# Kernel optimization log

Measured on AMD Instinct MI355X. Metric: run time of the kernel, lower is better.

The kernel has to match this reference:

```python
import jax, jax.numpy as jnp
import numpy as np

START_IDX = 1  # Offsets.GO
END_IDX = 2    # Offsets.EOS
NEG_INF = -10000.0


def setup_inputs() -> dict:
    key = jax.random.key(0)
    k1, k2, k3 = jax.random.split(key, 3)
    B, T, N = 256, 1024, 128
    unary = jax.random.normal(k1, (B, T, N), dtype=jnp.float32)
    trans = jax.random.normal(k2, (1, N, N), dtype=jnp.float32) * 0.1
    lengths = jax.random.randint(k3, (B,), 1, T + 1)
    return {"unary": unary, "trans": trans, "lengths": lengths}


def _forward_alg(unary_btn, trans, lengths):
    """CRF log-partition. unary_btn: [B,T,N], trans: [1,N,N], lengths: [B] -> [B]."""
    B, T, N = unary_btn.shape
    tr = trans[0]  # [N(cur), N(prev)]
    unary_tbn = jnp.transpose(unary_btn, (1, 0, 2))  # batch_first -> [T,B,N]

    init_alphas = jnp.full((B, N), NEG_INF, dtype=unary_btn.dtype)
    init_alphas = init_alphas.at[:, START_IDX].set(0.0)

    def step(alphas, inp):
        unary_t, t = inp  # unary_t: [B,N]
        # scores[b, i, j] = alphas[b, j] + trans[i, j] + unary_t[b, i]
        scores = alphas[:, None, :] + tr[None, :, :] + unary_t[:, :, None]
        new_alphas = jax.nn.logsumexp(scores, axis=2)  # [B,N]
        # only advance positions still inside the sequence
        alphas = jnp.where((t < lengths)[:, None], new_alphas, alphas)
        return alphas, None

    alphas, _ = jax.lax.scan(step, init_alphas, (unary_tbn, jnp.arange(T)))
    terminal = alphas + tr[END_IDX][None, :]  # trans[:, end_idx] row: [N]
    return jax.nn.logsumexp(terminal, axis=1)  # [B]


def reference(unary, trans, lengths):
    return _forward_alg(unary, trans, lengths)
```

## Files before the change

### kernel.cpp

```cpp
#include <hip/hip_runtime.h>

#define T_LEN 1024
#define NS    128
#define BT    16
#define G     16
#define SEG   32
#define SSH   5
#define NB    256

typedef __attribute__((ext_vector_type(8))) short short8;
typedef __attribute__((ext_vector_type(4))) short short4v;
typedef __attribute__((ext_vector_type(4))) float f32x4;

static __device__ __forceinline__ short f2bf(float f) {
    unsigned u = __builtin_bit_cast(unsigned, f);
    u = (u + 0x7fffu + ((u >> 16) & 1u)) >> 16;
    return (short)u;
}
static __device__ __forceinline__ float bf2f(short s) {
    unsigned u = ((unsigned)(unsigned short)s) << 16;
    return __builtin_bit_cast(float, u);
}
static __device__ __forceinline__ short f2bf_trunc(float f) {
    return (short)(__builtin_bit_cast(unsigned, f) >> 16);
}

__global__ __launch_bounds__(256, 1) void crf_seg(
        const float* __restrict__ unary, const float* __restrict__ trans,
        const int* __restrict__ lengths,
        float* __restrict__ yv, float* __restrict__ zv,
        float* __restrict__ cfv, float* __restrict__ cbv) {
    __shared__ __align__(16) short Fs[2][BT * NS];
    __shared__ __align__(16) float Us[2][BT * NS];
    __shared__ int tbS[BT], teS[BT];
    __shared__ int itersS;

    const int tid = threadIdx.x;
    const int g = blockIdx.x & (G - 1);
    const int u = blockIdx.x >> 4;
    const bool bwd = u >= (SEG - 1);
    const int s = bwd ? (u - (SEG - 2)) : u;
    const int w = tid >> 6, lane = tid & 63;
    const int quad = lane >> 4, bcol = lane & 15;
    const int sr = tid >> 4, sc = tid & 15;

    if (tid == 0) itersS = 0;
    if (tid < BT) {
        int L = lengths[g * BT + tid];
        tbS[tid] = (s * L) >> SSH;
        teS[tid] = ((s + 1) * L) >> SSH;
    }
    __syncthreads();
    if (tid < BT) atomicMax(&itersS, teS[tid] - tbS[tid]);

    const int tb = tbS[bcol], te = teS[bcol];
    const int nrec = te - tb - 1;
    const int s_tb = tbS[sr], s_te = teS[sr];

    short8 Ea[2][4];
    #pragma unroll
    for (int mt = 0; mt < 2; ++mt) {
        const int i = w * 32 + mt * 16 + bcol;
        #pragma unroll
        for (int kt = 0; kt < 4; ++kt) {
            short8 e;
            if (!bwd) {
                const float* tr = trans + (size_t)i * NS + kt * 32 + quad * 8;
                float4 x = *(const float4*)tr, y = *(const float4*)(tr + 4);
                e[0] = f2bf(__expf(x.x)); e[1] = f2bf(__expf(x.y));
                e[2] = f2bf(__expf(x.z)); e[3] = f2bf(__expf(x.w));
                e[4] = f2bf(__expf(y.x)); e[5] = f2bf(__expf(y.y));
                e[6] = f2bf(__expf(y.z)); e[7] = f2bf(__expf(y.w));
            } else {
                #pragma unroll
                for (int jj = 0; jj < 8; ++jj)
                    e[jj] = f2bf(__expf(trans[(size_t)(kt * 32 + quad * 8 + jj) * NS + i]));
            }
            Ea[mt][kt] = e;
        }
    }

    const float* ubase = unary + (size_t)(g * BT + sr) * T_LEN * NS + sc * 8;

    {
        float v[8];
        if (!bwd) {
            #pragma unroll
            for (int k = 0; k < 8; ++k)
                v[k] = (s == 0) ? ((sc * 8 + k == 1) ? 1.f : 0.f) : 1.f;
        } else {
            int ti = s_te - 1; if (ti < 0) ti = 0;
            const float* up = ubase + (size_t)ti * NS;
            float4 ua = *(const float4*)up, ub4 = *(const float4*)(up + 4);
            float uu[8] = {ua.x, ua.y, ua.z, ua.w, ub4.x, ub4.y, ub4.z, ub4.w};
            #pragma unroll
            for (int k = 0; k < 8; ++k) {
                float vv = (s == SEG - 1) ? __expf(trans[2 * NS + sc * 8 + k]) : 1.f;
                v[k] = __expf(uu[k]) * vv;
            }
        }
        short8 z;
        #pragma unroll
        for (int k = 0; k < 8; ++k) z[k] = f2bf(v[k]);
        *(short8*)&Fs[0][sr * NS + ((sc ^ sr) << 3)] = z;

        if (s_te == s_tb) {
            if (!bwd) {
                float* yp = yv + ((size_t)s * NB + g * BT + sr) * NS + sc * 8;
                #pragma unroll
                for (int k = 0; k < 8; ++k)
                    yp[k] = (s == 0) ? ((sc * 8 + k == 1) ? 1.f : 0.f) : 1.f;
                if (sc == 0) cfv[s * NB + g * BT + sr] = 0.f;
            } else {
                float* zp = zv + ((size_t)(s - 1) * NB + g * BT + sr) * NS + sc * 8;
                #pragma unroll
                for (int k = 0; k < 8; ++k) zp[k] = 1.f;
                if (sc == 0) cbv[(s - 1) * NB + g * BT + sr] = 0.f;
            }
        }
    }

    const int u_off0 = sr * NS + (((2 * sc) ^ (sr & 7)) << 2);
    const int u_off1 = sr * NS + (((2 * sc + 1) ^ (sr & 7)) << 2);
    #define T_OF(n) ({ int _t = bwd ? (s_te - 2 - (n)) : (s_tb + (n)); \
                       _t = _t < 0 ? 0 : (_t > T_LEN - 1 ? T_LEN - 1 : _t); _t; })
    float4 ra0, ra1;
    {
        int t = T_OF(0);
        ra0 = *(const float4*)(ubase + (size_t)t * NS);
        ra1 = *(const float4*)(ubase + (size_t)t * NS + 4);
        *(float4*)&Us[0][u_off0] = ra0;
        *(float4*)&Us[0][u_off1] = ra1;
        t = T_OF(1);
        ra0 = *(const float4*)(ubase + (size_t)t * NS);
        ra1 = *(const float4*)(ubase + (size_t)t * NS + 4);
    }
    __syncthreads();
    const int iters = itersS;

    int bfOff[4];
    #pragma unroll
    for (int kt = 0; kt < 4; ++kt) bfOff[kt] = bcol * NS + (((kt * 4 + quad) ^ bcol) << 3);
    const int s4Off = bcol * NS + (bcol << 3);
    const int ur0 = bcol * NS + (((w * 8 + quad) ^ (bcol & 7)) << 2);
    const int ur1 = bcol * NS + (((w * 8 + 4 + quad) ^ (bcol & 7)) << 2);
    const int c0 = w * 4 + (quad >> 1), half = (quad & 1) << 2;
    const int fw0 = bcol * NS + ((c0 ^ bcol) << 3) + half;
    const int fw1 = bcol * NS + (((c0 + 2) ^ bcol) << 3) + half;

    float C = 0.f;
    for (int n = 0; n < iters; ++n) {
        const int cur = n & 1, nxt = cur ^ 1;
        const short* fb = Fs[cur];
        short8 Bf0 = *(const short8*)&fb[bfOff[0]];
        short8 Bf1 = *(const short8*)&fb[bfOff[1]];
        short8 Bf2 = *(const short8*)&fb[bfOff[2]];
        short8 Bf3 = *(const short8*)&fb[bfOff[3]];
        short4v s4 = *(const short4v*)&fb[s4Off];
        float4 u0 = *(const float4*)&Us[cur][ur0];
        float4 u1 = *(const float4*)&Us[cur][ur1];

        *(float4*)&Us[nxt][u_off0] = ra0;
        *(float4*)&Us[nxt][u_off1] = ra1;
        {
            int t = T_OF(n + 2);
            ra0 = *(const float4*)(ubase + (size_t)t * NS);
            ra1 = *(const float4*)(ubase + (size_t)t * NS + 4);
        }

        f32x4 x0 = {0.f,0.f,0.f,0.f}, y0 = {0.f,0.f,0.f,0.f};
        f32x4 x1 = {0.f,0.f,0.f,0.f}, y1 = {0.f,0.f,0.f,0.f};
        x0 = __builtin_amdgcn_mfma_f32_16x16x32_bf16(Ea[0][0], Bf0, x0, 0, 0, 0);
        x1 = __builtin_amdgcn_mfma_f32_16x16x32_bf16(Ea[1][0], Bf0, x1, 0, 0, 0);
        y0 = __builtin_amdgcn_mfma_f32_16x16x32_bf16(Ea[0][2], Bf2, y0, 0, 0, 0);
        y1 = __builtin_amdgcn_mfma_f32_16x16x32_bf16(Ea[1][2], Bf2, y1, 0, 0, 0);
        x0 = __builtin_amdgcn_mfma_f32_16x16x32_bf16(Ea[0][1], Bf1, x0, 0, 0, 0);
        x1 = __builtin_amdgcn_mfma_f32_16x16x32_bf16(Ea[1][1], Bf1, x1, 0, 0, 0);
        y0 = __builtin_amdgcn_mfma_f32_16x16x32_bf16(Ea[0][3], Bf3, y0, 0, 0, 0);
        y1 = __builtin_amdgcn_mfma_f32_16x16x32_bf16(Ea[1][3], Bf3, y1, 0, 0, 0);
        f32x4 a0 = x0 + y0, a1 = x1 + y1;

        float sv = (bf2f(s4[0]) + bf2f(s4[1])) + (bf2f(s4[2]) + bf2f(s4[3]));
        float rs = __fdividef(1.f, sv);
        float logs = __logf(sv);
        float e0[4], e1[4];
        e0[0] = __expf(u0.x); e0[1] = __expf(u0.y); e0[2] = __expf(u0.z); e0[3] = __expf(u0.w);
        e1[0] = __expf(u1.x); e1[1] = __expf(u1.y); e1[2] = __expf(u1.z); e1[3] = __expf(u1.w);
        float fn0[4], fn1[4];
        #pragma unroll
        for (int r = 0; r < 4; ++r) {
            fn0[r] = a0[r] * e0[r] * rs;
            fn1[r] = a1[r] * e1[r] * rs;
        }

        if (n == nrec) {
            if (!bwd) {
                float* yp = yv + ((size_t)s * NB + g * BT + bcol) * NS;
                *(float4*)(yp + w * 32 + quad * 4)      = (float4){fn0[0], fn0[1], fn0[2], fn0[3]};
                *(float4*)(yp + w * 32 + 16 + quad * 4) = (float4){fn1[0], fn1[1], fn1[2], fn1[3]};
                if (tid < BT) cfv[s * NB + g * BT + tid] = C + logs;
            } else {
                float* zp = zv + ((size_t)(s - 1) * NB + g * BT + bcol) * NS;
                *(float4*)(zp + w * 32 + quad * 4)      = (float4){a0[0], a0[1], a0[2], a0[3]};
                *(float4*)(zp + w * 32 + 16 + quad * 4) = (float4){a1[0], a1[1], a1[2], a1[3]};
                if (tid < BT) cbv[(s - 1) * NB + g * BT + tid] = C;
            }
        }
        C += logs;

        short4v p0, p1;
        #pragma unroll
        for (int r = 0; r < 4; ++r) { p0[r] = f2bf_trunc(fn0[r]); p1[r] = f2bf_trunc(fn1[r]); }
        *(short4v*)&Fs[nxt][fw0] = p0;
        *(short4v*)&Fs[nxt][fw1] = p1;

        asm volatile("s_waitcnt lgkmcnt(0)" ::: "memory");
        __builtin_amdgcn_s_barrier();
    }
}

__global__ __launch_bounds__(64) void crf_combine(
        const float* __restrict__ yv, const float* __restrict__ zv,
        const float* __restrict__ cfv, const float* __restrict__ cbv,
        float* __restrict__ out) {
    const int b = blockIdx.x, lane = threadIdx.x;
    float acc = cfv[b];
    for (int s = 1; s <= SEG - 1; ++s) acc += cbv[(s - 1) * NB + b];
    float lg = 0.f;
    for (int s = 1; s <= SEG - 1; ++s) {
        const float* Z = zv + ((size_t)(s - 1) * NB + b) * NS;
        const float* Y = yv + ((size_t)(s - 1) * NB + b) * NS;
        float d = Z[lane] * Y[lane] + Z[lane + 64] * Y[lane + 64];
        #pragma unroll
        for (int off = 1; off < 64; off <<= 1) d += __shfl_xor(d, off, 64);
        lg += __logf(d);
    }
    for (int s = 1; s <= SEG - 2; ++s) {
        const float* Y = yv + ((size_t)s * NB + b) * NS;
        float t = Y[lane] + Y[lane + 64];
        #pragma unroll
        for (int off = 1; off < 64; off <<= 1) t += __shfl_xor(t, off, 64);
        lg -= __logf(t);
    }
    if (lane == 0) out[b] = acc + lg;
}

extern "C" void kernel_launch(void* const* d_in, const int* in_sizes, int n_in,
                              void* d_out, int out_size, void* d_ws, size_t ws_size,
                              hipStream_t stream) {
    const float* unary   = (const float*)d_in[0];
    const float* trans   = (const float*)d_in[1];
    const int*   lengths = (const int*)d_in[2];
    float* out = (float*)d_out;

    float* yv  = (float*)d_ws;
    float* zv  = yv + (size_t)(SEG - 1) * NB * NS;
    float* cfv = zv + (size_t)(SEG - 1) * NB * NS;
    float* cbv = cfv + (size_t)(SEG - 1) * NB;

    crf_seg<<<dim3(2 * (SEG - 1) * G), dim3(256), 0, stream>>>(
        unary, trans, lengths, yv, zv, cfv, cbv);
    crf_combine<<<dim3(NB), dim3(64), 0, stream>>>(yv, zv, cfv, cbv, out);
}
```

Baseline: 231.4 us.

## Load unary directly into MFMA output layout, dropping LDS staging buffer

New measurement: 228.9 us. No clear change (-1.1%).

```diff
diff --git a/kernel.cpp b/kernel.cpp
--- a/kernel.cpp
+++ b/kernel.cpp
@@ -25,13 +25,12 @@
     return (short)(__builtin_bit_cast(unsigned, f) >> 16);
 }
 
-__global__ __launch_bounds__(256, 1) void crf_seg(
+__global__ __launch_bounds__(256, 4) void crf_seg(
         const float* __restrict__ unary, const float* __restrict__ trans,
         const int* __restrict__ lengths,
         float* __restrict__ yv, float* __restrict__ zv,
         float* __restrict__ cfv, float* __restrict__ cbv) {
     __shared__ __align__(16) short Fs[2][BT * NS];
-    __shared__ __align__(16) float Us[2][BT * NS];
     __shared__ int tbS[BT], teS[BT];
     __shared__ int itersS;
 
@@ -80,9 +79,8 @@
         }
     }
 
-    const float* ubase = unary + (size_t)(g * BT + sr) * T_LEN * NS + sc * 8;
-
     {
+        const float* ubase = unary + (size_t)(g * BT + sr) * T_LEN * NS + sc * 8;
         float v[8];
         if (!bwd) {
             #pragma unroll
@@ -120,21 +118,16 @@
         }
     }
 
-    const int u_off0 = sr * NS + (((2 * sc) ^ (sr & 7)) << 2);
-    const int u_off1 = sr * NS + (((2 * sc + 1) ^ (sr & 7)) << 2);
-    #define T_OF(n) ({ int _t = bwd ? (s_te - 2 - (n)) : (s_tb + (n)); \
-                       _t = _t < 0 ? 0 : (_t > T_LEN - 1 ? T_LEN - 1 : _t); _t; })
-    float4 ra0, ra1;
-    {
-        int t = T_OF(0);
-        ra0 = *(const float4*)(ubase + (size_t)t * NS);
-        ra1 = *(const float4*)(ubase + (size_t)t * NS + 4);
-        *(float4*)&Us[0][u_off0] = ra0;
-        *(float4*)&Us[0][u_off1] = ra1;
-        t = T_OF(1);
-        ra0 = *(const float4*)(ubase + (size_t)t * NS);
-        ra1 = *(const float4*)(ubase + (size_t)t * NS + 4);
-    }
+    const float* uptr = unary + (size_t)(g * BT + bcol) * T_LEN * NS + (w * 32 + quad * 4);
+    #define T_OFB(nn) ({ int _t = bwd ? (te - 2 - (nn)) : (tb + (nn)); \
+                         _t = _t < 0 ? 0 : (_t > T_LEN - 1 ? T_LEN - 1 : _t); _t; })
+    float4 pA0, pA1, pB0, pB1;
+    { int t = T_OFB(0);
+      pA0 = *(const float4*)(uptr + (size_t)t * NS);
+      pA1 = *(const float4*)(uptr + (size_t)t * NS + 16); }
+    { int t = T_OFB(1);
+      pB0 = *(const float4*)(uptr + (size_t)t * NS);
+      pB1 = *(const float4*)(uptr + (size_t)t * NS + 16); }
     __syncthreads();
     const int iters = itersS;
 
@@ -142,81 +135,80 @@
     #pragma unroll
     for (int kt = 0; kt < 4; ++kt) bfOff[kt] = bcol * NS + (((kt * 4 + quad) ^ bcol) << 3);
     const int s4Off = bcol * NS + (bcol << 3);
-    const int ur0 = bcol * NS + (((w * 8 + quad) ^ (bcol & 7)) << 2);
-    const int ur1 = bcol * NS + (((w * 8 + 4 + quad) ^ (bcol & 7)) << 2);
     const int c0 = w * 4 + (quad >> 1), half = (quad & 1) << 2;
     const int fw0 = bcol * NS + ((c0 ^ bcol) << 3) + half;
     const int fw1 = bcol * NS + (((c0 + 2) ^ bcol) << 3) + half;
 
     float C = 0.f;
-    for (int n = 0; n < iters; ++n) {
-        const int cur = n & 1, nxt = cur ^ 1;
-        const short* fb = Fs[cur];
-        short8 Bf0 = *(const short8*)&fb[bfOff[0]];
-        short8 Bf1 = *(const short8*)&fb[bfOff[1]];
-        short8 Bf2 = *(const short8*)&fb[bfOff[2]];
-        short8 Bf3 = *(const short8*)&fb[bfOff[3]];
-        short4v s4 = *(const short4v*)&fb[s4Off];
-        float4 u0 = *(const float4*)&Us[cur][ur0];
-        float4 u1 = *(const float4*)&Us[cur][ur1];
-
-        *(float4*)&Us[nxt][u_off0] = ra0;
-        *(float4*)&Us[nxt][u_off1] = ra1;
-        {
-            int t = T_OF(n + 2);
-            ra0 = *(const float4*)(ubase + (size_t)t * NS);
-            ra1 = *(const float4*)(ubase + (size_t)t * NS + 4);
-        }
-
-        f32x4 x0 = {0.f,0.f,0.f,0.f}, y0 = {0.f,0.f,0.f,0.f};
-        f32x4 x1 = {0.f,0.f,0.f,0.f}, y1 = {0.f,0.f,0.f,0.f};
-        x0 = __builtin_amdgcn_mfma_f32_16x16x32_bf16(Ea[0][0], Bf0, x0, 0, 0, 0);
-        x1 = __builtin_amdgcn_mfma_f32_16x16x32_bf16(Ea[1][0], Bf0, x1, 0, 0, 0);
-        y0 = __builtin_amdgcn_mfma_f32_16x16x32_bf16(Ea[0][2], Bf2, y0, 0, 0, 0);
-        y1 = __builtin_amdgcn_mfma_f32_16x16x32_bf16(Ea[1][2], Bf2, y1, 0, 0, 0);
-        x0 = __builtin_amdgcn_mfma_f32_16x16x32_bf16(Ea[0][1], Bf1, x0, 0, 0, 0);
-        x1 = __builtin_amdgcn_mfma_f32_16x16x32_bf16(Ea[1][1], Bf1, x1, 0, 0, 0);
-        y0 = __builtin_amdgcn_mfma_f32_16x16x32_bf16(Ea[0][3], Bf3, y0, 0, 0, 0);
-        y1 = __builtin_amdgcn_mfma_f32_16x16x32_bf16(Ea[1][3], Bf3, y1, 0, 0, 0);
-        f32x4 a0 = x0 + y0, a1 = x1 + y1;
-
-        float sv = (bf2f(s4[0]) + bf2f(s4[1])) + (bf2f(s4[2]) + bf2f(s4[3]));
-        float rs = __fdividef(1.f, sv);
-        float logs = __logf(sv);
-        float e0[4], e1[4];
-        e0[0] = __expf(u0.x); e0[1] = __expf(u0.y); e0[2] = __expf(u0.z); e0[3] = __expf(u0.w);
-        e1[0] = __expf(u1.x); e1[1] = __expf(u1.y); e1[2] = __expf(u1.z); e1[3] = __expf(u1.w);
-        float fn0[4], fn1[4];
-        #pragma unroll
-        for (int r = 0; r < 4; ++r) {
-            fn0[r] = a0[r] * e0[r] * rs;
-            fn1[r] = a1[r] * e1[r] * rs;
-        }
-
-        if (n == nrec) {
-            if (!bwd) {
-                float* yp = yv + ((size_t)s * NB + g * BT + bcol) * NS;
-                *(float4*)(yp + w * 32 + quad * 4)      = (float4){fn0[0], fn0[1], fn0[2], fn0[3]};
-                *(float4*)(yp + w * 32 + 16 + quad * 4) = (float4){fn1[0], fn1[1], fn1[2], fn1[3]};
-                if (tid < BT) cfv[s * NB + g * BT + tid] = C + logs;
-            } else {
-                float* zp = zv + ((size_t)(s - 1) * NB + g * BT + bcol) * NS;
-                *(float4*)(zp + w * 32 + quad * 4)      = (float4){a0[0], a0[1], a0[2], a0[3]};
-                *(float4*)(zp + w * 32 + 16 + quad * 4) = (float4){a1[0], a1[1], a1[2], a1[3]};
-                if (tid < BT) cbv[(s - 1) * NB + g * BT + tid] = C;
-            }
-        }
-        C += logs;
-
-        short4v p0, p1;
-        #pragma unroll
-        for (int r = 0; r < 4; ++r) { p0[r] = f2bf_trunc(fn0[r]); p1[r] = f2bf_trunc(fn1[r]); }
-        *(short4v*)&Fs[nxt][fw0] = p0;
-        *(short4v*)&Fs[nxt][fw1] = p1;
-
-        asm volatile("s_waitcnt lgkmcnt(0)" ::: "memory");
-        __builtin_amdgcn_s_barrier();
-    }
+
+#define STEP(U0, U1) do {                                                         \
+    const int cur = n & 1, nxt = cur ^ 1;                                         \
+    const short* fb = Fs[cur];                                                    \
+    short8 Bf0 = *(const short8*)&fb[bfOff[0]];                                   \
+    short8 Bf1 = *(const short8*)&fb[bfOff[1]];                                   \
+    short8 Bf2 = *(const short8*)&fb[bfOff[2]];                                   \
+    short8 Bf3 = *(const short8*)&fb[bfOff[3]];                                   \
+    short4v s4 = *(const short4v*)&fb[s4Off];                                     \
+    float e0[4], e1[4];                                                           \
+    e0[0] = __expf(U0.x); e0[1] = __expf(U0.y);                                   \
+    e0[2] = __expf(U0.z); e0[3] = __expf(U0.w);                                   \
+    e1[0] = __expf(U1.x); e1[1] = __expf(U1.y);                                   \
+    e1[2] = __expf(U1.z); e1[3] = __expf(U1.w);                                   \
+    { int t = T_OFB(n + 2);                                                       \
+      U0 = *(const float4*)(uptr + (size_t)t * NS);                               \
+      U1 = *(const float4*)(uptr + (size_t)t * NS + 16); }                        \
+    f32x4 x0 = {0.f,0.f,0.f,0.f}, y0 = {0.f,0.f,0.f,0.f};                         \
+    f32x4 x1 = {0.f,0.f,0.f,0.f}, y1 = {0.f,0.f,0.f,0.f};                         \
+    x0 = __builtin_amdgcn_mfma_f32_16x16x32_bf16(Ea[0][0], Bf0, x0, 0, 0, 0);     \
+    x1 = __builtin_amdgcn_mfma_f32_16x16x32_bf16(Ea[1][0], Bf0, x1, 0, 0, 0);     \
+    y0 = __builtin_amdgcn_mfma_f32_16x16x32_bf16(Ea[0][2], Bf2, y0, 0, 0, 0);     \
+    y1 = __builtin_amdgcn_mfma_f32_16x16x32_bf16(Ea[1][2], Bf2, y1, 0, 0, 0);     \
+    x0 = __builtin_amdgcn_mfma_f32_16x16x32_bf16(Ea[0][1], Bf1, x0, 0, 0, 0);     \
+    x1 = __builtin_amdgcn_mfma_f32_16x16x32_bf16(Ea[1][1], Bf1, x1, 0, 0, 0);     \
+    y0 = __builtin_amdgcn_mfma_f32_16x16x32_bf16(Ea[0][3], Bf3, y0, 0, 0, 0);     \
+    y1 = __builtin_amdgcn_mfma_f32_16x16x32_bf16(Ea[1][3], Bf3, y1, 0, 0, 0);     \
+    f32x4 a0 = x0 + y0, a1 = x1 + y1;                                             \
+    float sv = (bf2f(s4[0]) + bf2f(s4[1])) + (bf2f(s4[2]) + bf2f(s4[3]));         \
+    float rs = __fdividef(1.f, sv);                                               \
+    float logs = __logf(sv);                                                      \
+    float fn0[4], fn1[4];                                                         \
+    fn0[0] = a0[0]*e0[0]*rs; fn0[1] = a0[1]*e0[1]*rs;                             \
+    fn0[2] = a0[2]*e0[2]*rs; fn0[3] = a0[3]*e0[3]*rs;                             \
+    fn1[0] = a1[0]*e1[0]*rs; fn1[1] = a1[1]*e1[1]*rs;                             \
+    fn1[2] = a1[2]*e1[2]*rs; fn1[3] = a1[3]*e1[3]*rs;                             \
+    if (n == nrec) {                                                              \
+        if (!bwd) {              \
+            float* yp = yv + ((size_t)s * NB + g * BT + bcol) * NS;               \
+            *(float4*)(yp + w * 32 + quad * 4)      = (float4){fn0[0], fn0[1], fn0[2], fn0[3]}; \
+            *(float4*)(yp + w * 32 + 16 + quad * 4) = (float4){fn1[0], fn1[1], fn1[2], fn1[3]}; \
+            if (tid < BT) cfv[s * NB + g * BT + tid] = C + logs;                  \
+        } else {                  \
+            float* zp = zv + ((size_t)(s - 1) * NB + g * BT + bcol) * NS;         \
+            *(float4*)(zp + w * 32 + quad * 4)      = (float4){a0[0], a0[1], a0[2], a0[3]}; \
+            *(float4*)(zp + w * 32 + 16 + quad * 4) = (float4){a1[0], a1[1], a1[2], a1[3]}; \
+            if (tid < BT) cbv[(s - 1) * NB + g * BT + tid] = C;                   \
+        }                                                                         \
+    }                                                                             \
+    C += logs;                                                                    \
+    short4v p0, p1;                                                               \
+    p0[0] = f2bf_trunc(fn0[0]); p0[1] = f2bf_trunc(fn0[1]);                       \
+    p0[2] = f2bf_trunc(fn0[2]); p0[3] = f2bf_trunc(fn0[3]);                       \
+    p1[0] = f2bf_trunc(fn1[0]); p1[1] = f2bf_trunc(fn1[1]);                       \
+    p1[2] = f2bf_trunc(fn1[2]); p1[3] = f2bf_trunc(fn1[3]);                       \
+    *(short4v*)&Fs[nxt][fw0] = p0;                                                \
+    *(short4v*)&Fs[nxt][fw1] = p1;                                                \
+     \
+    asm volatile("s_waitcnt lgkmcnt(0)" ::: "memory");                            \
+    __builtin_amdgcn_s_barrier();                                                 \
+} while (0)
+
+    for (int n = 0; n < iters; ) {
+        STEP(pA0, pA1); ++n;
+        if (n >= iters) break;
+        STEP(pB0, pB1); ++n;
+    }
+#undef STEP
+#undef T_OFB
 }
 
 __global__ __launch_bounds__(64) void crf_combine(
```

## Split sequence into 128 segments with shared LDS exp(unary) and merged fwd/bwd blocks

Applied to the files above, without the earlier changes.

Measured after the change: 253.7 us. 1.1x slower.

```diff
diff --git a/kernel.cpp b/kernel.cpp
--- a/kernel.cpp
+++ b/kernel.cpp
@@ -4,8 +4,9 @@
 #define NS    128
 #define BT    16
 #define G     16
-#define SEG   32
-#define SSH   5
+#define SEG   128
+#define SSH   7
+#define ST    8
 #define NB    256
 
 typedef __attribute__((ext_vector_type(8))) short short8;
@@ -25,209 +26,270 @@
     return (short)(__builtin_bit_cast(unsigned, f) >> 16);
 }
 
-__global__ __launch_bounds__(256, 1) void crf_seg(
+__global__ __launch_bounds__(256, 4) void crf_seg(
         const float* __restrict__ unary, const float* __restrict__ trans,
         const int* __restrict__ lengths,
         float* __restrict__ yv, float* __restrict__ zv,
         float* __restrict__ cfv, float* __restrict__ cbv) {
-    __shared__ __align__(16) short Fs[2][BT * NS];
-    __shared__ __align__(16) float Us[2][BT * NS];
+    __shared__ __align__(16) short Fs[BT * NS];
+    __shared__ __align__(16) short EU[ST * BT * NS];
     __shared__ int tbS[BT], teS[BT];
-    __shared__ int itersS;
 
     const int tid = threadIdx.x;
     const int g = blockIdx.x & (G - 1);
-    const int u = blockIdx.x >> 4;
-    const bool bwd = u >= (SEG - 1);
-    const int s = bwd ? (u - (SEG - 2)) : u;
+    const int s = blockIdx.x >> 4;
     const int w = tid >> 6, lane = tid & 63;
     const int quad = lane >> 4, bcol = lane & 15;
-    const int sr = tid >> 4, sc = tid & 15;
-
-    if (tid == 0) itersS = 0;
+
     if (tid < BT) {
         int L = lengths[g * BT + tid];
         tbS[tid] = (s * L) >> SSH;
         teS[tid] = ((s + 1) * L) >> SSH;
     }
+    {
+        short8 z = {0, 0, 0, 0, 0, 0, 0, 0};
+        #pragma unroll
+        for (int k = 0; k < 8; ++k) *(short8*)&EU[tid * 64 + k * 8] = z;
+    }
     __syncthreads();
-    if (tid < BT) atomicMax(&itersS, teS[tid] - tbS[tid]);
 
     const int tb = tbS[bcol], te = teS[bcol];
-    const int nrec = te - tb - 1;
-    const int s_tb = tbS[sr], s_te = teS[sr];
-
-    short8 Ea[2][4];
+    const int slen = te - tb;
+    const int nrec = slen - 1;
+    int iters = 0;
     #pragma unroll
-    for (int mt = 0; mt < 2; ++mt) {
-        const int i = w * 32 + mt * 16 + bcol;
-        #pragma unroll
-        for (int kt = 0; kt < 4; ++kt) {
-            short8 e;
-            if (!bwd) {
-                const float* tr = trans + (size_t)i * NS + kt * 32 + quad * 8;
-                float4 x = *(const float4*)tr, y = *(const float4*)(tr + 4);
+    for (int b = 0; b < BT; ++b) {
+        int d = teS[b] - tbS[b];
+        iters = d > iters ? d : iters;
+    }
+    const int slc = slen > 0 ? slen - 1 : 0;
+
+    {
+        const int sb = tid >> 4, rr = (tid >> 1) & 7, hh = tid & 1;
+        const int sl = teS[sb] - tbS[sb];
+        if (rr < sl) {
+            const float* src = unary + ((size_t)(g * BT + sb) * T_LEN + tbS[sb] + rr) * NS + hh * 64;
+            #pragma unroll
+            for (int k8 = 0; k8 < 8; ++k8) {
+                float4 x = *(const float4*)(src + k8 * 8);
+                float4 y = *(const float4*)(src + k8 * 8 + 4);
+                short8 e;
                 e[0] = f2bf(__expf(x.x)); e[1] = f2bf(__expf(x.y));
                 e[2] = f2bf(__expf(x.z)); e[3] = f2bf(__expf(x.w));
                 e[4] = f2bf(__expf(y.x)); e[5] = f2bf(__expf(y.y));
                 e[6] = f2bf(__expf(y.z)); e[7] = f2bf(__expf(y.w));
-            } else {
+                const int c8 = hh * 8 + k8;
+                *(short8*)&EU[rr * (BT * NS) + sb * NS + (((c8 ^ sb) & 15) << 3)] = e;
+            }
+        }
+    }
+
+    short8 Ea[2][4];
+    if (s < SEG - 1) {
+        #pragma unroll
+        for (int mt = 0; mt < 2; ++mt) {
+            const int i = w * 32 + mt * 16 + bcol;
+            #pragma unroll
+            for (int kt = 0; kt < 4; ++kt) {
+                const float* tr = trans + (size_t)i * NS + kt * 32 + quad * 8;
+                float4 x = *(const float4*)tr, y = *(const float4*)(tr + 4);
+                short8 e;
+                e[0] = f2bf(__expf(x.x)); e[1] = f2bf(__expf(x.y));
+                e[2] = f2bf(__expf(x.z)); e[3] = f2bf(__expf(x.w));
+                e[4] = f2bf(__expf(y.x)); e[5] = f2bf(__expf(y.y));
+                e[6] = f2bf(__expf(y.z)); e[7] = f2bf(__expf(y.w));
+                Ea[mt][kt] = e;
+            }
+        }
+    }
+
+    {
+        const int sr = tid >> 4, sc = tid & 15;
+        const int sl = teS[sr] - tbS[sr];
+        short8 z;
+        #pragma unroll
+        for (int k = 0; k < 8; ++k)
+            z[k] = f2bf((s == 0) ? ((sc * 8 + k == 1) ? 1.f : 0.f) : 1.f);
+        *(short8*)&Fs[sr * NS + ((sc ^ sr) << 3)] = z;
+
+        if (sl == 0 && s < SEG - 1) {
+            float* yp = yv + ((size_t)s * NB + g * BT + sr) * NS + sc * 8;
+            #pragma unroll
+            for (int k = 0; k < 8; ++k)
+                yp[k] = (s == 0) ? ((sc * 8 + k == 1) ? 1.f : 0.f) : 1.f;
+            if (sc == 0) cfv[s * NB + g * BT + sr] = 0.f;
+        }
+    }
+    __syncthreads();
+
+    int bfOff[4];
+    #pragma unroll
+    for (int kt = 0; kt < 4; ++kt) bfOff[kt] = bcol * NS + (((kt * 4 + quad) ^ bcol) << 3);
+    const int s4Off = bcol * NS + (bcol << 3);
+    const int c0 = w * 4 + (quad >> 1), halfo = (quad & 1) << 2;
+    const int fw0 = bcol * NS + ((c0 ^ bcol) << 3) + halfo;
+    const int fw1 = bcol * NS + (((c0 + 2) ^ bcol) << 3) + halfo;
+
+#define LGKM_BAR() do { asm volatile("s_waitcnt lgkmcnt(0)" ::: "memory"); \
+                        __builtin_amdgcn_s_barrier(); } while (0)
+
+    if (s < SEG - 1) {
+        float C = 0.f;
+        for (int n = 0; n < iters; ++n) {
+            short8 Bf0 = *(const short8*)&Fs[bfOff[0]];
+            short8 Bf1 = *(const short8*)&Fs[bfOff[1]];
+            short8 Bf2 = *(const short8*)&Fs[bfOff[2]];
+            short8 Bf3 = *(const short8*)&Fs[bfOff[3]];
+            short4v s4 = *(const short4v*)&Fs[s4Off];
+            const int er = n < slen ? n : slc;
+            short4v ev0 = *(const short4v*)&EU[er * (BT * NS) + fw0];
+            short4v ev1 = *(const short4v*)&EU[er * (BT * NS) + fw1];
+            LGKM_BAR();
+
+            float sv = (bf2f(s4[0]) + bf2f(s4[1])) + (bf2f(s4[2]) + bf2f(s4[3]));
+            float rs = __fdividef(1.f, sv);
+            float logs = __logf(sv);
+
+            f32x4 x0 = {0.f,0.f,0.f,0.f}, y0 = {0.f,0.f,0.f,0.f};
+            f32x4 x1 = {0.f,0.f,0.f,0.f}, y1 = {0.f,0.f,0.f,0.f};
+            x0 = __builtin_amdgcn_mfma_f32_16x16x32_bf16(Ea[0][0], Bf0, x0, 0, 0, 0);
+            x1 = __builtin_amdgcn_mfma_f32_16x16x32_bf16(Ea[1][0], Bf0, x1, 0, 0, 0);
+            y0 = __builtin_amdgcn_mfma_f32_16x16x32_bf16(Ea[0][2], Bf2, y0, 0, 0, 0);
+            y1 = __builtin_amdgcn_mfma_f32_16x16x32_bf16(Ea[1][2], Bf2, y1, 0, 0, 0);
+            x0 = __builtin_amdgcn_mfma_f32_16x16x32_bf16(Ea[0][1], Bf1, x0, 0, 0, 0);
+            x1 = __builtin_amdgcn_mfma_f32_16x16x32_bf16(Ea[1][1], Bf1, x1, 0, 0, 0);
+            y0 = __builtin_amdgcn_mfma_f32_16x16x32_bf16(Ea[0][3], Bf3, y0, 0, 0, 0);
+            y1 = __builtin_amdgcn_mfma_f32_16x16x32_bf16(Ea[1][3], Bf3, y1, 0, 0, 0);
+            f32x4 a0 = x0 + y0, a1 = x1 + y1;
+
+            float fn0[4], fn1[4];
+            #pragma unroll
+            for (int r = 0; r < 4; ++r) {
+                fn0[r] = a0[r] * bf2f(ev0[r]) * rs;
+                fn1[r] = a1[r] * bf2f(ev1[r]) * rs;
+            }
+
+            if (n == nrec) {
+                float* yp = yv + ((size_t)s * NB + g * BT + bcol) * NS;
+                *(float4*)(yp + w * 32 + quad * 4)      = (float4){fn0[0], fn0[1], fn0[2], fn0[3]};
+                *(float4*)(yp + w * 32 + 16 + quad * 4) = (float4){fn1[0], fn1[1], fn1[2], fn1[3]};
+                if (tid < BT) cfv[s * NB + g * BT + tid] = C + logs;
+            }
+            C += logs;
+
+            short4v p0, p1;
+            #pragma unroll
+            for (int r = 0; r < 4; ++r) { p0[r] = f2bf_trunc(fn0[r]); p1[r] = f2bf_trunc(fn1[r]); }
+            *(short4v*)&Fs[fw0] = p0;
+            *(short4v*)&Fs[fw1] = p1;
+            LGKM_BAR();
+        }
+    }
+
+    if (s != 0) {
+        if (iters > 0) {
+            #pragma unroll
+            for (int mt = 0; mt < 2; ++mt) {
+                const int i = w * 32 + mt * 16 + bcol;
                 #pragma unroll
-                for (int jj = 0; jj < 8; ++jj)
-                    e[jj] = f2bf(__expf(trans[(size_t)(kt * 32 + quad * 8 + jj) * NS + i]));
-            }
-            Ea[mt][kt] = e;
-        }
-    }
-
-    const float* ubase = unary + (size_t)(g * BT + sr) * T_LEN * NS + sc * 8;
-
-    {
-        float v[8];
-        if (!bwd) {
-            #pragma unroll
-            for (int k = 0; k < 8; ++k)
-                v[k] = (s == 0) ? ((sc * 8 + k == 1) ? 1.f : 0.f) : 1.f;
-        } else {
-            int ti = s_te - 1; if (ti < 0) ti = 0;
-            const float* up = ubase + (size_t)ti * NS;
-            float4 ua = *(const float4*)up, ub4 = *(const float4*)(up + 4);
-            float uu[8] = {ua.x, ua.y, ua.z, ua.w, ub4.x, ub4.y, ub4.z, ub4.w};
-            #pragma unroll
-            for (int k = 0; k < 8; ++k) {
-                float vv = (s == SEG - 1) ? __expf(trans[2 * NS + sc * 8 + k]) : 1.f;
-                v[k] = __expf(uu[k]) * vv;
-            }
-        }
-        short8 z;
-        #pragma unroll
-        for (int k = 0; k < 8; ++k) z[k] = f2bf(v[k]);
-        *(short8*)&Fs[0][sr * NS + ((sc ^ sr) << 3)] = z;
-
-        if (s_te == s_tb) {
-            if (!bwd) {
-                float* yp = yv + ((size_t)s * NB + g * BT + sr) * NS + sc * 8;
-                #pragma unroll
-                for (int k = 0; k < 8; ++k)
-                    yp[k] = (s == 0) ? ((sc * 8 + k == 1) ? 1.f : 0.f) : 1.f;
-                if (sc == 0) cfv[s * NB + g * BT + sr] = 0.f;
-            } else {
+                for (int kt = 0; kt < 4; ++kt) {
+                    short8 e;
+                    #pragma unroll
+                    for (int jj = 0; jj < 8; ++jj)
+                        e[jj] = f2bf(__expf(trans[(size_t)(kt * 32 + quad * 8 + jj) * NS + i]));
+                    Ea[mt][kt] = e;
+                }
+            }
+        }
+        {
+            const int sr = tid >> 4, sc = tid & 15;
+            const int sl = teS[sr] - tbS[sr];
+            if (sl == 0) {
                 float* zp = zv + ((size_t)(s - 1) * NB + g * BT + sr) * NS + sc * 8;
                 #pragma unroll
                 for (int k = 0; k < 8; ++k) zp[k] = 1.f;
                 if (sc == 0) cbv[(s - 1) * NB + g * BT + sr] = 0.f;
-            }
-        }
-    }
-
-    const int u_off0 = sr * NS + (((2 * sc) ^ (sr & 7)) << 2);
-    const int u_off1 = sr * NS + (((2 * sc + 1) ^ (sr & 7)) << 2);
-    #define T_OF(n) ({ int _t = bwd ? (s_te - 2 - (n)) : (s_tb + (n)); \
-                       _t = _t < 0 ? 0 : (_t > T_LEN - 1 ? T_LEN - 1 : _t); _t; })
-    float4 ra0, ra1;
-    {
-        int t = T_OF(0);
-        ra0 = *(const float4*)(ubase + (size_t)t * NS);
-        ra1 = *(const float4*)(ubase + (size_t)t * NS + 4);
-        *(float4*)&Us[0][u_off0] = ra0;
-        *(float4*)&Us[0][u_off1] = ra1;
-        t = T_OF(1);
-        ra0 = *(const float4*)(ubase + (size_t)t * NS);
-        ra1 = *(const float4*)(ubase + (size_t)t * NS + 4);
-    }
-    __syncthreads();
-    const int iters = itersS;
-
-    int bfOff[4];
-    #pragma unroll
-    for (int kt = 0; kt < 4; ++kt) bfOff[kt] = bcol * NS + (((kt * 4 + quad) ^ bcol) << 3);
-    const int s4Off = bcol * NS + (bcol << 3);
-    const int ur0 = bcol * NS + (((w * 8 + quad) ^ (bcol & 7)) << 2);
-    const int ur1 = bcol * NS + (((w * 8 + 4 + quad) ^ (bcol & 7)) << 2);
-    const int c0 = w * 4 + (quad >> 1), half = (quad & 1) << 2;
-    const int fw0 = bcol * NS + ((c0 ^ bcol) << 3) + half;
-    const int fw1 = bcol * NS + (((c0 + 2) ^ bcol) << 3) + half;
-
-    float C = 0.f;
-    for (int n = 0; n < iters; ++n) {
-        const int cur = n & 1, nxt = cur ^ 1;
-        const short* fb = Fs[cur];
-        short8 Bf0 = *(const short8*)&fb[bfOff[0]];
-        short8 Bf1 = *(const short8*)&fb[bfOff[1]];
-        short8 Bf2 = *(const short8*)&fb[bfOff[2]];
-        short8 Bf3 = *(const short8*)&fb[bfOff[3]];
-        short4v s4 = *(const short4v*)&fb[s4Off];
-        float4 u0 = *(const float4*)&Us[cur][ur0];
-        float4 u1 = *(const float4*)&Us[cur][ur1];
-
-        *(float4*)&Us[nxt][u_off0] = ra0;
-        *(float4*)&Us[nxt][u_off1] = ra1;
-        {
-            int t = T_OF(n + 2);
-            ra0 = *(const float4*)(ubase + (size_t)t * NS);
-            ra1 = *(const float4*)(ubase + (size_t)t * NS + 4);
-        }
-
-        f32x4 x0 = {0.f,0.f,0.f,0.f}, y0 = {0.f,0.f,0.f,0.f};
-        f32x4 x1 = {0.f,0.f,0.f,0.f}, y1 = {0.f,0.f,0.f,0.f};
-        x0 = __builtin_amdgcn_mfma_f32_16x16x32_bf16(Ea[0][0], Bf0, x0, 0, 0, 0);
-        x1 = __builtin_amdgcn_mfma_f32_16x16x32_bf16(Ea[1][0], Bf0, x1, 0, 0, 0);
-        y0 = __builtin_amdgcn_mfma_f32_16x16x32_bf16(Ea[0][2], Bf2, y0, 0, 0, 0);
-        y1 = __builtin_amdgcn_mfma_f32_16x16x32_bf16(Ea[1][2], Bf2, y1, 0, 0, 0);
-        x0 = __builtin_amdgcn_mfma_f32_16x16x32_bf16(Ea[0][1], Bf1, x0, 0, 0, 0);
-        x1 = __builtin_amdgcn_mfma_f32_16x16x32_bf16(Ea[1][1], Bf1, x1, 0, 0, 0);
-        y0 = __builtin_amdgcn_mfma_f32_16x16x32_bf16(Ea[0][3], Bf3, y0, 0, 0, 0);
-        y1 = __builtin_amdgcn_mfma_f32_16x16x32_bf16(Ea[1][3], Bf3, y1, 0, 0, 0);
-        f32x4 a0 = x0 + y0, a1 = x1 + y1;
-
-        float sv = (bf2f(s4[0]) + bf2f(s4[1])) + (bf2f(s4[2]) + bf2f(s4[3]));
-        float rs = __fdividef(1.f, sv);
-        float logs = __logf(sv);
-        float e0[4], e1[4];
-        e0[0] = __expf(u0.x); e0[1] = __expf(u0.y); e0[2] = __expf(u0.z); e0[3] = __expf(u0.w);
-        e1[0] = __expf(u1.x); e1[1] = __expf(u1.y); e1[2] = __expf(u1.z); e1[3] = __expf(u1.w);
-        float fn0[4], fn1[4];
-        #pragma unroll
-        for (int r = 0; r < 4; ++r) {
-            fn0[r] = a0[r] * e0[r] * rs;
-            fn1[r] = a1[r] * e1[r] * rs;
-        }
-
-        if (n == nrec) {
-            if (!bwd) {
-                float* yp = yv + ((size_t)s * NB + g * BT + bcol) * NS;
-                *(float4*)(yp + w * 32 + quad * 4)      = (float4){fn0[0], fn0[1], fn0[2], fn0[3]};
-                *(float4*)(yp + w * 32 + 16 + quad * 4) = (float4){fn1[0], fn1[1], fn1[2], fn1[3]};
-                if (tid < BT) cfv[s * NB + g * BT + tid] = C + logs;
+                short8 z;
+                #pragma unroll
+                for (int k = 0; k < 8; ++k) z[k] = f2bf(1.f);
+                *(short8*)&Fs[sr * NS + ((sc ^ sr) << 3)] = z;
             } else {
+                short8 eu8 = *(const short8*)&EU[(sl - 1) * (BT * NS) + sr * NS + (((sc ^ sr) & 15) << 3)];
+                short8 z;
+                #pragma unroll
+                for (int k = 0; k < 8; ++k) {
+                    float vv = (s == SEG - 1) ? __expf(trans[2 * NS + sc * 8 + k]) : 1.f;
+                    z[k] = f2bf(bf2f(eu8[k]) * vv);
+                }
+                *(short8*)&Fs[sr * NS + ((sc ^ sr) << 3)] = z;
+            }
+        }
+        __syncthreads();
+
+        float Cb = 0.f;
+        for (int m = 0; m < iters; ++m) {
+            short8 Bf0 = *(const short8*)&Fs[bfOff[0]];
+            short8 Bf1 = *(const short8*)&Fs[bfOff[1]];
+            short8 Bf2 = *(const short8*)&Fs[bfOff[2]];
+            short8 Bf3 = *(const short8*)&Fs[bfOff[3]];
+            short4v s4 = *(const short4v*)&Fs[s4Off];
+            int r = slen - 2 - m; r = r < 0 ? 0 : r;
+            short4v ev0 = *(const short4v*)&EU[r * (BT * NS) + fw0];
+            short4v ev1 = *(const short4v*)&EU[r * (BT * NS) + fw1];
+            LGKM_BAR();
+
+            float sv = (bf2f(s4[0]) + bf2f(s4[1])) + (bf2f(s4[2]) + bf2f(s4[3]));
+            float rs = __fdividef(1.f, sv);
+            float logs = __logf(sv);
+
+            f32x4 x0 = {0.f,0.f,0.f,0.f}, y0 = {0.f,0.f,0.f,0.f};
+            f32x4 x1 = {0.f,0.f,0.f,0.f}, y1 = {0.f,0.f,0.f,0.f};
+            x0 = __builtin_amdgcn_mfma_f32_16x16x32_bf16(Ea[0][0], Bf0, x0, 0, 0, 0);
+            x1 = __builtin_amdgcn_mfma_f32_16x16x32_bf16(Ea[1][0], Bf0, x1, 0, 0, 0);
+            y0 = __builtin_amdgcn_mfma_f32_16x16x32_bf16(Ea[0][2], Bf2, y0, 0, 0, 0);
+            y1 = __builtin_amdgcn_mfma_f32_16x16x32_bf16(Ea[1][2], Bf2, y1, 0, 0, 0);
+            x0 = __builtin_amdgcn_mfma_f32_16x16x32_bf16(Ea[0][1], Bf1, x0, 0, 0, 0);
+            x1 = __builtin_amdgcn_mfma_f32_16x16x32_bf16(Ea[1][1], Bf1, x1, 0, 0, 0);
+            y0 = __builtin_amdgcn_mfma_f32_16x16x32_bf16(Ea[0][3], Bf3, y0, 0, 0, 0);
+            y1 = __builtin_amdgcn_mfma_f32_16x16x32_bf16(Ea[1][3], Bf3, y1, 0, 0, 0);
+            f32x4 a0 = x0 + y0, a1 = x1 + y1;
+
+            if (m == nrec) {
                 float* zp = zv + ((size_t)(s - 1) * NB + g * BT + bcol) * NS;
                 *(float4*)(zp + w * 32 + quad * 4)      = (float4){a0[0], a0[1], a0[2], a0[3]};
                 *(float4*)(zp + w * 32 + 16 + quad * 4) = (float4){a1[0], a1[1], a1[2], a1[3]};
-                if (tid < BT) cbv[(s - 1) * NB + g * BT + tid] = C;
-            }
-        }
-        C += logs;
-
-        short4v p0, p1;
-        #pragma unroll
-        for (int r = 0; r < 4; ++r) { p0[r] = f2bf_trunc(fn0[r]); p1[r] = f2bf_trunc(fn1[r]); }
-        *(short4v*)&Fs[nxt][fw0] = p0;
-        *(short4v*)&Fs[nxt][fw1] = p1;
-
-        asm volatile("s_waitcnt lgkmcnt(0)" ::: "memory");
-        __builtin_amdgcn_s_barrier();
-    }
-}
-
-__global__ __launch_bounds__(64) void crf_combine(
+                if (tid < BT) cbv[(s - 1) * NB + g * BT + tid] = Cb;
+            }
+
+            float fn0[4], fn1[4];
+            #pragma unroll
+            for (int r2 = 0; r2 < 4; ++r2) {
+                fn0[r2] = a0[r2] * bf2f(ev0[r2]) * rs;
+                fn1[r2] = a1[r2] * bf2f(ev1[r2]) * rs;
+            }
+            Cb += logs;
+
+            short4v p0, p1;
+            #pragma unroll
+            for (int r2 = 0; r2 < 4; ++r2) { p0[r2] = f2bf_trunc(fn0[r2]); p1[r2] = f2bf_trunc(fn1[r2]); }
+            *(short4v*)&Fs[fw0] = p0;
+            *(short4v*)&Fs[fw1] = p1;
+            LGKM_BAR();
+        }
+    }
+#undef LGKM_BAR
+}
+
+__global__ __launch_bounds__(256) void crf_combine(
         const float* __restrict__ yv, const float* __restrict__ zv,
         const float* __restrict__ cfv, const float* __restrict__ cbv,
         float* __restrict__ out) {
-    const int b = blockIdx.x, lane = threadIdx.x;
-    float acc = cfv[b];
-    for (int s = 1; s <= SEG - 1; ++s) acc += cbv[(s - 1) * NB + b];
+    __shared__ float part[4];
+    const int b = blockIdx.x, tid = threadIdx.x;
+    const int w = tid >> 6, lane = tid & 63;
     float lg = 0.f;
-    for (int s = 1; s <= SEG - 1; ++s) {
+    for (int s = 1 + w; s <= SEG - 1; s += 4) lg += cbv[(s - 1) * NB + b];
+    for (int s = 1 + w; s <= SEG - 1; s += 4) {
         const float* Z = zv + ((size_t)(s - 1) * NB + b) * NS;
         const float* Y = yv + ((size_t)(s - 1) * NB + b) * NS;
         float d = Z[lane] * Y[lane] + Z[lane + 64] * Y[lane + 64];
@@ -235,14 +297,16 @@
         for (int off = 1; off < 64; off <<= 1) d += __shfl_xor(d, off, 64);
         lg += __logf(d);
     }
-    for (int s = 1; s <= SEG - 2; ++s) {
+    for (int s = 1 + w; s <= SEG - 2; s += 4) {
         const float* Y = yv + ((size_t)s * NB + b) * NS;
         float t = Y[lane] + Y[lane + 64];
         #pragma unroll
         for (int off = 1; off < 64; off <<= 1) t += __shfl_xor(t, off, 64);
         lg -= __logf(t);
     }
-    if (lane == 0) out[b] = acc + lg;
+    if (lane == 0) part[w] = lg;
+    __syncthreads();
+    if (tid == 0) out[b] = cfv[b] + ((part[0] + part[1]) + (part[2] + part[3]));
 }
 
 extern "C" void kernel_launch(void* const* d_in, const int* in_sizes, int n_in,
@@ -258,7 +322,7 @@
     float* cfv = zv + (size_t)(SEG - 1) * NB * NS;
     float* cbv = cfv + (size_t)(SEG - 1) * NB;
 
-    crf_seg<<<dim3(2 * (SEG - 1) * G), dim3(256), 0, stream>>>(
+    crf_seg<<<dim3(SEG * G), dim3(256), 0, stream>>>(
         unary, trans, lengths, yv, zv, cfv, cbv);
-    crf_combine<<<dim3(NB), dim3(64), 0, stream>>>(yv, zv, cfv, cbv, out);
-}
+    crf_combine<<<dim3(NB), dim3(256), 0, stream>>>(yv, zv, cfv, cbv, out);
+}
```
